# Optimization experiments

Hardware: AMD Instinct MI355X
Metric: run time of the kernel (lower is better)

The kernel has to match this reference:

```python
import jax, jax.numpy as jnp
import numpy as np

N_NODES = 8192
IN_FEATS, H_FEATS, NUM_CLASSES = 512, 256, 16


def _glorot(key, shape):
    fan_in, fan_out = shape[0], shape[1]
    limit = float(np.sqrt(6.0 / (fan_in + fan_out)))
    return jax.random.uniform(key, shape, jnp.float32, -limit, limit)


def setup_inputs() -> dict:
    key = jax.random.key(0)
    ks = jax.random.split(key, 16)
    return {
        "x": jax.random.normal(ks[0], (N_NODES, IN_FEATS), jnp.float32),
        "w1": _glorot(ks[1], (IN_FEATS, H_FEATS)), "b1": jnp.zeros((H_FEATS,), jnp.float32),
        "w2": _glorot(ks[2], (H_FEATS, H_FEATS)), "b2": jnp.zeros((H_FEATS,), jnp.float32),
        "w3": _glorot(ks[3], (H_FEATS, 32)),      "b3": jnp.zeros((32,), jnp.float32),
        "t": _glorot(ks[4], (1, 1)), "theta": _glorot(ks[5], (1, 1)),
        "gw1": _glorot(ks[6], (32, 16)), "gb1": jnp.zeros((16,), jnp.float32),
        "gw2": _glorot(ks[7], (16, 8)),  "gb2": jnp.zeros((8,), jnp.float32),
        "lw1": _glorot(ks[8], (8, 16)),  "lb1": jnp.zeros((16,), jnp.float32),
        "lw2": _glorot(ks[9], (16, NUM_CLASSES)), "lb2": jnp.zeros((NUM_CLASSES,), jnp.float32),
    }


def _pairwise_dist(h):
    # Euclidean cdist(h, h): [N, N], stable sqrt with zero subgradient at d=0
    sq = jnp.sum(h * h, axis=1)
    d2 = jnp.maximum(sq[:, None] + sq[None, :] - 2.0 * (h @ h.T), 0.0)
    return jnp.where(d2 > 0.0, jnp.sqrt(jnp.where(d2 > 0.0, d2, 1.0)), 0.0)


def reference(x, w1, b1, w2, b2, w3, b3, t, theta, gw1, gb1, gw2, gb2, lw1, lb1, lw2, lb2):
    n = x.shape[0]
    # MLP encoder (dropout is eval-mode identity)
    h = jax.nn.relu(x @ w1 + b1)
    h = jax.nn.relu(h @ w2 + b2)
    h = h @ w3 + b3                                  # [N, 32]
    # latent dense graph: A = sigmoid(t * (cdist + theta)); all entries > 0 -> fully dense graph
    A = jax.nn.sigmoid(t[0, 0] * (_pairwise_dist(h) + theta[0, 0]))   # [N, N]
    inv_deg = 1.0 / n                                # norm='right', in-degree == N for dense graph
    # GraphConv: dst aggregates sum_src A[src,dst] * (h[src] @ W) then right-normalizes
    h = jax.nn.relu((A.T @ (h @ gw1)) * inv_deg + gb1)   # [N, 16]
    h = jax.nn.relu((A.T @ (h @ gw2)) * inv_deg + gb2)   # [N, 8]
    h = jax.nn.relu(h @ lw1 + lb1)
    return h @ lw2 + lb2                             # [N, num_classes]
```

## Files before the change

kernel.cpp:

```cpp
#include <hip/hip_runtime.h>

typedef __attribute__((ext_vector_type(8))) short short8;
typedef __attribute__((ext_vector_type(4))) float f32x4;
typedef __attribute__((ext_vector_type(4))) unsigned short u16x4;
typedef unsigned short u16;
typedef unsigned int u32;

#define MFMA16 __builtin_amdgcn_mfma_f32_16x16x32_bf16

__device__ __forceinline__ u16 f2bf(float f) {
    u32 u = __builtin_bit_cast(u32, f);
    return (u16)((u + 0x7FFFu + ((u >> 16) & 1u)) >> 16);
}

__device__ __forceinline__ void split2(float f, u16& hi, u16& lo) {
    u32 u = __builtin_bit_cast(u32, f);
    hi = (u16)(u >> 16);
    float hf = __builtin_bit_cast(float, u & 0xFFFF0000u);
    float r = f - hf;
    lo = (u16)(__builtin_bit_cast(u32, r) >> 16);
}

__device__ __forceinline__ int swzA(int row, int slot) {
    return row * 64 + ((slot ^ ((row >> 1) & 3)) << 4);
}

__global__ void __launch_bounds__(256) k_tr(const float* __restrict__ w, float* __restrict__ wt,
                                            int K, int N) {
    int idx = blockIdx.x * 256 + threadIdx.x;
    if (idx >= K * N) return;
    int k = idx / N, n = idx - k * N;
    wt[n * K + k] = w[idx];
}

template <int K, int BN, bool RELU>
__global__ void __launch_bounds__(256, 2) k_gemm(const float* __restrict__ A,
                                                 const float* __restrict__ Bt,
                                                 const float* __restrict__ bias,
                                                 float* __restrict__ C, const int N) {
    constexpr int NT = BN / 16;
    __shared__ __align__(16) char smem[16384];
    char* const Ah = smem;
    char* const Al = smem + 4096;
    char* const Bh = smem + 8192;
    char* const Bl = smem + 12288;
    const int tid = threadIdx.x, lane = tid & 63, w = tid >> 6;
    const int frow = lane & 15, fg = lane >> 4;
    const int m0 = blockIdx.x * 64, n0 = blockIdx.y * BN;
    const int srow = tid >> 2, sc = tid & 3;
    const int swa = swzA(srow, sc);
    const bool doB = (BN == 64) || (tid < 128);
    const float* gA = A + (m0 + srow) * K + sc * 8;
    const float* gB = Bt + (n0 + srow) * K + sc * 8;

    f32x4 acc[NT];
    float bv[NT];
#pragma unroll
    for (int nt = 0; nt < NT; nt++) {
        acc[nt] = {0.f, 0.f, 0.f, 0.f};
        bv[nt] = bias[n0 + nt * 16 + frow];
    }
    const int fra = swzA(w * 16 + frow, fg);
    int frb[NT];
#pragma unroll
    for (int nt = 0; nt < NT; nt++) frb[nt] = swzA(nt * 16 + frow, fg);

    for (int k0 = 0; k0 < K; k0 += 32) {
        f32x4 a0 = *(const f32x4*)(gA + k0);
        f32x4 a1 = *(const f32x4*)(gA + k0 + 4);
        f32x4 b0 = {0.f, 0.f, 0.f, 0.f}, b1 = {0.f, 0.f, 0.f, 0.f};
        if (doB) {
            b0 = *(const f32x4*)(gB + k0);
            b1 = *(const f32x4*)(gB + k0 + 4);
        }
        __syncthreads();
        {
            short8 ah8, al8;
#pragma unroll
            for (int i = 0; i < 4; i++) { u16 hh, ll; split2(a0[i], hh, ll); ah8[i] = (short)hh; al8[i] = (short)ll; }
#pragma unroll
            for (int i = 0; i < 4; i++) { u16 hh, ll; split2(a1[i], hh, ll); ah8[4 + i] = (short)hh; al8[4 + i] = (short)ll; }
            *(short8*)(Ah + swa) = ah8;
            *(short8*)(Al + swa) = al8;
        }
        if (doB) {
            short8 bh8, bl8;
#pragma unroll
            for (int i = 0; i < 4; i++) { u16 hh, ll; split2(b0[i], hh, ll); bh8[i] = (short)hh; bl8[i] = (short)ll; }
#pragma unroll
            for (int i = 0; i < 4; i++) { u16 hh, ll; split2(b1[i], hh, ll); bh8[4 + i] = (short)hh; bl8[4 + i] = (short)ll; }
            *(short8*)(Bh + swa) = bh8;
            *(short8*)(Bl + swa) = bl8;
        }
        __syncthreads();
        const short8 afh = *(const short8*)(Ah + fra);
        const short8 afl = *(const short8*)(Al + fra);
#pragma unroll
        for (int nt = 0; nt < NT; nt++) {
            const short8 bfh = *(const short8*)(Bh + frb[nt]);
            const short8 bfl = *(const short8*)(Bl + frb[nt]);
            acc[nt] = MFMA16(afh, bfh, acc[nt], 0, 0, 0);
            acc[nt] = MFMA16(afh, bfl, acc[nt], 0, 0, 0);
            acc[nt] = MFMA16(afl, bfh, acc[nt], 0, 0, 0);
        }
    }
#pragma unroll
    for (int nt = 0; nt < NT; nt++) {
#pragma unroll
        for (int r = 0; r < 4; r++) {
            float v = acc[nt][r] + bv[nt];
            if (RELU) v = fmaxf(v, 0.f);
            C[(m0 + w * 16 + fg * 4 + r) * N + (n0 + nt * 16 + frow)] = v;
        }
    }
}

__global__ void __launch_bounds__(256) k_post(const float* __restrict__ H,
                                              const float* __restrict__ gw1,
                                              u16* __restrict__ hhi, u16* __restrict__ hlo,
                                              float* __restrict__ sqv, u16* __restrict__ B1t) {
    __shared__ float gs[512];
    const int tid = threadIdx.x;
    gs[tid] = gw1[tid];
    gs[tid + 256] = gw1[tid + 256];
    __syncthreads();
    const int j = blockIdx.x * 256 + tid;
    float h[32];
#pragma unroll
    for (int q = 0; q < 8; q++) {
        f32x4 v = *(const f32x4*)(H + j * 32 + q * 4);
        h[q * 4 + 0] = v[0]; h[q * 4 + 1] = v[1]; h[q * 4 + 2] = v[2]; h[q * 4 + 3] = v[3];
    }
    float s = 0.f;
#pragma unroll
    for (int k = 0; k < 32; k++) s = fmaf(h[k], h[k], s);
    sqv[j] = s;
#pragma unroll
    for (int q = 0; q < 4; q++) {
        short8 vh, vl;
#pragma unroll
        for (int e = 0; e < 8; e++) {
            u16 hh, ll;
            split2(h[q * 8 + e], hh, ll);
            vh[e] = (short)hh; vl[e] = (short)ll;
        }
        *(short8*)(hhi + j * 32 + q * 8) = vh;
        *(short8*)(hlo + j * 32 + q * 8) = vl;
    }
    const float inv = 0.0001220703125f;
#pragma unroll
    for (int f = 0; f < 16; f++) {
        float a = 0.f;
#pragma unroll
        for (int k = 0; k < 32; k++) a = fmaf(h[k], gs[k * 16 + f], a);
        B1t[f * 8192 + j] = f2bf(a * inv);
    }
}

__global__ void __launch_bounds__(256, 2) k_agg(const u16* __restrict__ hhi,
                                                const u16* __restrict__ hlo,
                                                const float* __restrict__ sqv,
                                                const u16* __restrict__ Bt,
                                                float* __restrict__ P,
                                                const float* __restrict__ tp,
                                                const float* __restrict__ thp) {
    __shared__ __align__(16) char smem[25088];
    const int tid = threadIdx.x;
    const int lane = tid & 63;
    const int w = tid >> 6;
    const int frow = lane & 15, fg = lane >> 4;
    const int dstbase = blockIdx.x * 64;
    const int chunk = blockIdx.y;
    const float t = tp[0], th = thp[0];
    const float c1 = -t * 1.44269504088896340736f;
    const float c0 = c1 * th;

    char* const hdh_p = smem;
    char* const hdl_p = smem + 4096;
    char* const hsh_p = smem + 8192;
    char* const hsl_p = smem + 12288;
    float* const sqd = (float*)(smem + 16384);
    float* const sqs = (float*)(smem + 16640);
    char* const astr = smem + 16896 + w * 2048;

    const int srow = tid >> 2, sc = tid & 3;
    const int swa = swzA(srow, sc);

    {
        short8 vh = *(const short8*)(hhi + (dstbase + srow) * 32 + sc * 8);
        short8 vl = *(const short8*)(hlo + (dstbase + srow) * 32 + sc * 8);
        *(short8*)(hdh_p + swa) = vh;
        *(short8*)(hdl_p + swa) = vl;
        if (tid < 64) sqd[tid] = sqv[dstbase + tid];
    }
    __syncthreads();

    const int fra = swzA(w * 16 + frow, fg);
    const short8 hdh = *(const short8*)(hdh_p + fra);
    const short8 hdl = *(const short8*)(hdl_p + fra);
    const float sq_i = sqd[w * 16 + frow];
    const int il = w * 16 + frow;

    int hsfa[4], aw_off[4], ard[2];
#pragma unroll
    for (int jj = 0; jj < 4; jj++) hsfa[jj] = swzA(jj * 16 + frow, fg);
#pragma unroll
    for (int jj = 0; jj < 4; jj++)
        aw_off[jj] = frow * 128 + (((2 * jj + (fg >> 1)) ^ (frow & 7)) << 4) + ((fg & 1) << 3);
#pragma unroll
    for (int ks = 0; ks < 2; ks++) ard[ks] = frow * 128 + (((4 * ks + fg) ^ (frow & 7)) << 4);

    f32x4 outacc = {0.f, 0.f, 0.f, 0.f};
    const u16* bgp = Bt + frow * 8192;

    for (int jt = chunk * 16; jt < chunk * 16 + 16; ++jt) {
        const int jbase = jt * 64;
        const short8 bf0 = *(const short8*)(bgp + jbase + fg * 8);
        const short8 bf1 = *(const short8*)(bgp + jbase + 32 + fg * 8);
        const short8 vh = *(const short8*)(hhi + (jbase + srow) * 32 + sc * 8);
        const short8 vl = *(const short8*)(hlo + (jbase + srow) * 32 + sc * 8);
        const int il_cmp = (jbase == dstbase) ? il : -1;
        __syncthreads();
        *(short8*)(hsh_p + swa) = vh;
        *(short8*)(hsl_p + swa) = vl;
        if (tid < 64) sqs[tid] = sqv[jbase + tid];
        __syncthreads();

        short8 hsh[4], hsl[4];
#pragma unroll
        for (int jj = 0; jj < 4; jj++) {
            hsh[jj] = *(const short8*)(hsh_p + hsfa[jj]);
            hsl[jj] = *(const short8*)(hsl_p + hsfa[jj]);
        }
        f32x4 sacc[4];
#pragma unroll
        for (int jj = 0; jj < 4; jj++) {
            f32x4 z = {0.f, 0.f, 0.f, 0.f};
            z = MFMA16(hsh[jj], hdh, z, 0, 0, 0);
            z = MFMA16(hsh[jj], hdl, z, 0, 0, 0);
            z = MFMA16(hsl[jj], hdh, z, 0, 0, 0);
            sacc[jj] = z;
        }
#pragma unroll
        for (int jj = 0; jj < 4; jj++) {
            u16x4 av;
#pragma unroll
            for (int r = 0; r < 4; r++) {
                const int jl = jj * 16 + fg * 4 + r;
                const float sqj = sqs[jl];
                float d2 = fmaf(sacc[jj][r], -2.f, sq_i + sqj);
                d2 = fmaxf(d2, 0.f);
                float d = __builtin_amdgcn_sqrtf(d2);
                if (jl == il_cmp) d = 0.f;
                const float zz = fmaf(d, c1, c0);
                const float aa = __builtin_amdgcn_rcpf(1.f + __builtin_amdgcn_exp2f(zz));
                av[r] = f2bf(aa);
            }
            *(u16x4*)(astr + aw_off[jj]) = av;
        }
        const short8 af0 = *(const short8*)(astr + ard[0]);
        const short8 af1 = *(const short8*)(astr + ard[1]);
        outacc = MFMA16(af0, bf0, outacc, 0, 0, 0);
        outacc = MFMA16(af1, bf1, outacc, 0, 0, 0);
    }
#pragma unroll
    for (int r = 0; r < 4; r++) {
        const int ig = dstbase + w * 16 + fg * 4 + r;
        P[(chunk * 8192 + ig) * 16 + frow] = outacc[r];
    }
}

__global__ void __launch_bounds__(256) k_reduce1(const float* __restrict__ P,
                                                 const float* __restrict__ gw2,
                                                 const float* __restrict__ gb1,
                                                 u16* __restrict__ B2t) {
    __shared__ float gs[128];
    const int tid = threadIdx.x;
    if (tid < 128) gs[tid] = gw2[tid];
    __syncthreads();
    const int j = blockIdx.x * 256 + tid;
    float g[16];
#pragma unroll
    for (int q = 0; q < 4; q++) {
        f32x4 v = *(const f32x4*)(P + j * 16 + q * 4);
        g[q * 4 + 0] = v[0]; g[q * 4 + 1] = v[1]; g[q * 4 + 2] = v[2]; g[q * 4 + 3] = v[3];
    }
#pragma unroll
    for (int c = 1; c < 8; c++) {
#pragma unroll
        for (int q = 0; q < 4; q++) {
            f32x4 v = *(const f32x4*)(P + (c * 8192 + j) * 16 + q * 4);
            g[q * 4 + 0] += v[0]; g[q * 4 + 1] += v[1]; g[q * 4 + 2] += v[2]; g[q * 4 + 3] += v[3];
        }
    }
#pragma unroll
    for (int f = 0; f < 16; f++) g[f] = fmaxf(g[f] + gb1[f], 0.f);
    const float inv = 0.0001220703125f;
#pragma unroll
    for (int f2 = 0; f2 < 8; f2++) {
        float a = 0.f;
#pragma unroll
        for (int k = 0; k < 16; k++) a = fmaf(g[k], gs[k * 8 + f2], a);
        B2t[f2 * 8192 + j] = f2bf(a * inv);
    }
#pragma unroll
    for (int f2 = 8; f2 < 16; f2++) B2t[f2 * 8192 + j] = 0;
}

__global__ void __launch_bounds__(256) k_final(const float* __restrict__ P,
                                               const float* __restrict__ gb2,
                                               const float* __restrict__ lw1,
                                               const float* __restrict__ lb1,
                                               const float* __restrict__ lw2,
                                               const float* __restrict__ lb2,
                                               float* __restrict__ out) {
    __shared__ float s1[128], s2[256];
    const int tid = threadIdx.x;
    if (tid < 128) s1[tid] = lw1[tid];
    s2[tid] = lw2[tid];
    __syncthreads();
    const int j = blockIdx.x * 256 + tid;
    float g[8];
#pragma unroll
    for (int q = 0; q < 2; q++) {
        f32x4 v = *(const f32x4*)(P + j * 16 + q * 4);
        g[q * 4 + 0] = v[0]; g[q * 4 + 1] = v[1]; g[q * 4 + 2] = v[2]; g[q * 4 + 3] = v[3];
    }
#pragma unroll
    for (int c = 1; c < 8; c++) {
#pragma unroll
        for (int q = 0; q < 2; q++) {
            f32x4 v = *(const f32x4*)(P + (c * 8192 + j) * 16 + q * 4);
            g[q * 4 + 0] += v[0]; g[q * 4 + 1] += v[1]; g[q * 4 + 2] += v[2]; g[q * 4 + 3] += v[3];
        }
    }
#pragma unroll
    for (int f = 0; f < 8; f++) g[f] = fmaxf(g[f] + gb2[f], 0.f);
    float l1[16];
#pragma unroll
    for (int f = 0; f < 16; f++) {
        float a = lb1[f];
#pragma unroll
        for (int k = 0; k < 8; k++) a = fmaf(g[k], s1[k * 16 + f], a);
        l1[f] = fmaxf(a, 0.f);
    }
#pragma unroll
    for (int q = 0; q < 4; q++) {
        f32x4 v;
#pragma unroll
        for (int e = 0; e < 4; e++) {
            const int f = q * 4 + e;
            float a = lb2[f];
#pragma unroll
            for (int k = 0; k < 16; k++) a = fmaf(l1[k], s2[k * 16 + f], a);
            v[e] = a;
        }
        *(f32x4*)(out + j * 16 + q * 4) = v;
    }
}

extern "C" void kernel_launch(void* const* d_in, const int* in_sizes, int n_in,
                              void* d_out, int out_size, void* d_ws, size_t ws_size,
                              hipStream_t stream) {
    (void)in_sizes; (void)n_in; (void)out_size; (void)ws_size;
    const float* x   = (const float*)d_in[0];
    const float* w1  = (const float*)d_in[1];
    const float* b1  = (const float*)d_in[2];
    const float* w2  = (const float*)d_in[3];
    const float* b2  = (const float*)d_in[4];
    const float* w3  = (const float*)d_in[5];
    const float* b3  = (const float*)d_in[6];
    const float* t   = (const float*)d_in[7];
    const float* th  = (const float*)d_in[8];
    const float* gw1 = (const float*)d_in[9];
    const float* gb1 = (const float*)d_in[10];
    const float* gw2 = (const float*)d_in[11];
    const float* gb2 = (const float*)d_in[12];
    const float* lw1 = (const float*)d_in[13];
    const float* lb1 = (const float*)d_in[14];
    const float* lw2 = (const float*)d_in[15];
    const float* lb2 = (const float*)d_in[16];

    char* ws = (char*)d_ws;
    float* wt1 = (float*)(ws + 0);
    float* wt2 = (float*)(ws + 524288);
    float* wt3 = (float*)(ws + 786432);
    float* H1  = (float*)(ws + 819200);
    float* P   = (float*)(ws + 819200);
    float* H2  = (float*)(ws + 9207808);
    float* H   = (float*)(ws + 17596416);
    u16*   hhi = (u16*)(ws + 18644992);
    u16*   hlo = (u16*)(ws + 19169280);
    float* sqv = (float*)(ws + 19693568);
    u16*   B1t = (u16*)(ws + 19726336);
    u16*   B2t = (u16*)(ws + 19988480);

    k_tr<<<(512 * 256 + 255) / 256, 256, 0, stream>>>(w1, wt1, 512, 256);
    k_tr<<<(256 * 256 + 255) / 256, 256, 0, stream>>>(w2, wt2, 256, 256);
    k_tr<<<(256 * 32 + 255) / 256, 256, 0, stream>>>(w3, wt3, 256, 32);

    k_gemm<512, 64, true ><<<dim3(128, 4), 256, 0, stream>>>(x,  wt1, b1, H1, 256);
    k_gemm<256, 64, true ><<<dim3(128, 4), 256, 0, stream>>>(H1, wt2, b2, H2, 256);
    k_gemm<256, 32, false><<<dim3(128, 1), 256, 0, stream>>>(H2, wt3, b3, H, 32);

    k_post<<<32, 256, 0, stream>>>(H, gw1, hhi, hlo, sqv, B1t);

    k_agg<<<dim3(128, 8), 256, 0, stream>>>(hhi, hlo, sqv, B1t, P, t, th);
    k_reduce1<<<32, 256, 0, stream>>>(P, gw2, gb1, B2t);
    k_agg<<<dim3(128, 8), 256, 0, stream>>>(hhi, hlo, sqv, B2t, P, t, th);
    k_final<<<32, 256, 0, stream>>>(P, gb2, lw1, lb1, lw2, lb2, (float*)d_out);
}
```

Before: 140.1 us.

## Drop LDS staging, pre-split weights/activations to bf16 pairs, double aggregation chunks

The GEMM kernels no longer stage tiles through LDS with barriers. They load MFMA fragments directly from global memory, using weights pre-split into hi/lo bf16 by the transpose kernel and intermediate activations written already split. The aggregation kernel likewise reads source features straight from global memory without syncthreads and packs probabilities with v_cvt_pk_bf16_f32. The source dimension is split into 16 chunks instead of 8 for more parallelism, at the cost of a larger partial-sum reduction and more uncoalesced, L2-dependent global reads.

```diff
diff --git a/kernel.cpp b/kernel.cpp
--- a/kernel.cpp
+++ b/kernel.cpp
@@ -2,11 +2,14 @@
 
 typedef __attribute__((ext_vector_type(8))) short short8;
 typedef __attribute__((ext_vector_type(4))) float f32x4;
-typedef __attribute__((ext_vector_type(4))) unsigned short u16x4;
+typedef __attribute__((ext_vector_type(2))) unsigned int u32x2;
 typedef unsigned short u16;
 typedef unsigned int u32;
 
 #define MFMA16 __builtin_amdgcn_mfma_f32_16x16x32_bf16
+
+constexpr int NCH = 16;
+constexpr int NJT = 8192 / 64 / NCH;
 
 __device__ __forceinline__ u16 f2bf(float f) {
     u32 u = __builtin_bit_cast(u32, f);
@@ -21,38 +24,28 @@
     lo = (u16)(__builtin_bit_cast(u32, r) >> 16);
 }
 
-__device__ __forceinline__ int swzA(int row, int slot) {
-    return row * 64 + ((slot ^ ((row >> 1) & 3)) << 4);
-}
-
-__global__ void __launch_bounds__(256) k_tr(const float* __restrict__ w, float* __restrict__ wt,
-                                            int K, int N) {
+__global__ void __launch_bounds__(256) k_trs(const float* __restrict__ w, u16* __restrict__ wthi,
+                                             u16* __restrict__ wtlo, int K, int N) {
     int idx = blockIdx.x * 256 + threadIdx.x;
     if (idx >= K * N) return;
     int k = idx / N, n = idx - k * N;
-    wt[n * K + k] = w[idx];
-}
-
-template <int K, int BN, bool RELU>
-__global__ void __launch_bounds__(256, 2) k_gemm(const float* __restrict__ A,
-                                                 const float* __restrict__ Bt,
-                                                 const float* __restrict__ bias,
-                                                 float* __restrict__ C, const int N) {
-    constexpr int NT = BN / 16;
-    __shared__ __align__(16) char smem[16384];
-    char* const Ah = smem;
-    char* const Al = smem + 4096;
-    char* const Bh = smem + 8192;
-    char* const Bl = smem + 12288;
+    u16 hh, ll;
+    split2(w[idx], hh, ll);
+    wthi[n * K + k] = hh;
+    wtlo[n * K + k] = ll;
+}
+
+template <int K, int NT, bool RELU, bool AF32, bool OUTSPLIT>
+__global__ void __launch_bounds__(256) k_gemm(const float* __restrict__ Af,
+                                              const u16* __restrict__ Ahi, const u16* __restrict__ Alo,
+                                              const u16* __restrict__ Bthi, const u16* __restrict__ Btlo,
+                                              const float* __restrict__ bias,
+                                              float* __restrict__ Cf, u16* __restrict__ Chi,
+                                              u16* __restrict__ Clo, const int N) {
     const int tid = threadIdx.x, lane = tid & 63, w = tid >> 6;
     const int frow = lane & 15, fg = lane >> 4;
-    const int m0 = blockIdx.x * 64, n0 = blockIdx.y * BN;
-    const int srow = tid >> 2, sc = tid & 3;
-    const int swa = swzA(srow, sc);
-    const bool doB = (BN == 64) || (tid < 128);
-    const float* gA = A + (m0 + srow) * K + sc * 8;
-    const float* gB = Bt + (n0 + srow) * K + sc * 8;
-
+    const int m0 = blockIdx.x * 64, n0 = blockIdx.y * NT * 16;
+    const int arow = m0 + w * 16 + frow;
     f32x4 acc[NT];
     float bv[NT];
 #pragma unroll
@@ -60,48 +53,26 @@
         acc[nt] = {0.f, 0.f, 0.f, 0.f};
         bv[nt] = bias[n0 + nt * 16 + frow];
     }
-    const int fra = swzA(w * 16 + frow, fg);
-    int frb[NT];
-#pragma unroll
-    for (int nt = 0; nt < NT; nt++) frb[nt] = swzA(nt * 16 + frow, fg);
-
     for (int k0 = 0; k0 < K; k0 += 32) {
-        f32x4 a0 = *(const f32x4*)(gA + k0);
-        f32x4 a1 = *(const f32x4*)(gA + k0 + 4);
-        f32x4 b0 = {0.f, 0.f, 0.f, 0.f}, b1 = {0.f, 0.f, 0.f, 0.f};
-        if (doB) {
-            b0 = *(const f32x4*)(gB + k0);
-            b1 = *(const f32x4*)(gB + k0 + 4);
-        }
-        __syncthreads();
-        {
-            short8 ah8, al8;
-#pragma unroll
-            for (int i = 0; i < 4; i++) { u16 hh, ll; split2(a0[i], hh, ll); ah8[i] = (short)hh; al8[i] = (short)ll; }
-#pragma unroll
-            for (int i = 0; i < 4; i++) { u16 hh, ll; split2(a1[i], hh, ll); ah8[4 + i] = (short)hh; al8[4 + i] = (short)ll; }
-            *(short8*)(Ah + swa) = ah8;
-            *(short8*)(Al + swa) = al8;
-        }
-        if (doB) {
-            short8 bh8, bl8;
-#pragma unroll
-            for (int i = 0; i < 4; i++) { u16 hh, ll; split2(b0[i], hh, ll); bh8[i] = (short)hh; bl8[i] = (short)ll; }
-#pragma unroll
-            for (int i = 0; i < 4; i++) { u16 hh, ll; split2(b1[i], hh, ll); bh8[4 + i] = (short)hh; bl8[4 + i] = (short)ll; }
-            *(short8*)(Bh + swa) = bh8;
-            *(short8*)(Bl + swa) = bl8;
-        }
-        __syncthreads();
-        const short8 afh = *(const short8*)(Ah + fra);
-        const short8 afl = *(const short8*)(Al + fra);
+        short8 ah, al;
+        if constexpr (AF32) {
+            const f32x4 a0 = *(const f32x4*)(Af + arow * K + k0 + fg * 8);
+            const f32x4 a1 = *(const f32x4*)(Af + arow * K + k0 + fg * 8 + 4);
+#pragma unroll
+            for (int i = 0; i < 4; i++) { u16 hh, ll; split2(a0[i], hh, ll); ah[i] = (short)hh; al[i] = (short)ll; }
+#pragma unroll
+            for (int i = 0; i < 4; i++) { u16 hh, ll; split2(a1[i], hh, ll); ah[4 + i] = (short)hh; al[4 + i] = (short)ll; }
+        } else {
+            ah = *(const short8*)(Ahi + arow * K + k0 + fg * 8);
+            al = *(const short8*)(Alo + arow * K + k0 + fg * 8);
+        }
 #pragma unroll
         for (int nt = 0; nt < NT; nt++) {
-            const short8 bfh = *(const short8*)(Bh + frb[nt]);
-            const short8 bfl = *(const short8*)(Bl + frb[nt]);
-            acc[nt] = MFMA16(afh, bfh, acc[nt], 0, 0, 0);
-            acc[nt] = MFMA16(afh, bfl, acc[nt], 0, 0, 0);
-            acc[nt] = MFMA16(afl, bfh, acc[nt], 0, 0, 0);
+            const short8 bh = *(const short8*)(Bthi + (n0 + nt * 16 + frow) * K + k0 + fg * 8);
+            const short8 bl = *(const short8*)(Btlo + (n0 + nt * 16 + frow) * K + k0 + fg * 8);
+            acc[nt] = MFMA16(ah, bh, acc[nt], 0, 0, 0);
+            acc[nt] = MFMA16(ah, bl, acc[nt], 0, 0, 0);
+            acc[nt] = MFMA16(al, bh, acc[nt], 0, 0, 0);
         }
     }
 #pragma unroll
@@ -110,7 +81,15 @@
         for (int r = 0; r < 4; r++) {
             float v = acc[nt][r] + bv[nt];
             if (RELU) v = fmaxf(v, 0.f);
-            C[(m0 + w * 16 + fg * 4 + r) * N + (n0 + nt * 16 + frow)] = v;
+            const int row = m0 + w * 16 + fg * 4 + r, col = n0 + nt * 16 + frow;
+            if constexpr (OUTSPLIT) {
+                u16 hh, ll;
+                split2(v, hh, ll);
+                Chi[row * N + col] = hh;
+                Clo[row * N + col] = ll;
+            } else {
+                Cf[row * N + col] = v;
+            }
         }
     }
 }
@@ -157,111 +136,87 @@
     }
 }
 
-__global__ void __launch_bounds__(256, 2) k_agg(const u16* __restrict__ hhi,
-                                                const u16* __restrict__ hlo,
-                                                const float* __restrict__ sqv,
-                                                const u16* __restrict__ Bt,
-                                                float* __restrict__ P,
-                                                const float* __restrict__ tp,
-                                                const float* __restrict__ thp) {
-    __shared__ __align__(16) char smem[25088];
-    const int tid = threadIdx.x;
-    const int lane = tid & 63;
-    const int w = tid >> 6;
+template <bool DIAG>
+__device__ __forceinline__ void ew_pack(char* astr, int awoff, const f32x4 s, const f32x4 sq4,
+                                        float sq_i, float c0, float c1, int jloc, int il) {
+    float p[4];
+#pragma unroll
+    for (int r = 0; r < 4; r++) {
+        float d2 = fmaf(s[r], -2.f, sq_i + sq4[r]);
+        d2 = fmaxf(d2, 0.f);
+        float d = __builtin_amdgcn_sqrtf(d2);
+        if (DIAG) {
+            if (jloc + r == il) d = 0.f;
+        }
+        const float z = fmaf(d, c1, c0);
+        p[r] = __builtin_amdgcn_rcpf(1.f + __builtin_amdgcn_exp2f(z));
+    }
+    u32 w0, w1;
+    asm("v_cvt_pk_bf16_f32 %0, %1, %2" : "=v"(w0) : "v"(p[0]), "v"(p[1]));
+    asm("v_cvt_pk_bf16_f32 %0, %1, %2" : "=v"(w1) : "v"(p[2]), "v"(p[3]));
+    u32x2 pk = {w0, w1};
+    *(u32x2*)(astr + awoff) = pk;
+}
+
+__global__ void __launch_bounds__(256) k_agg(const u16* __restrict__ hhi, const u16* __restrict__ hlo,
+                                             const float* __restrict__ sqv, const u16* __restrict__ Bt,
+                                             float* __restrict__ P,
+                                             const float* __restrict__ tp, const float* __restrict__ thp) {
+    __shared__ __align__(16) char astr_all[8192];
+    const int tid = threadIdx.x, lane = tid & 63, w = tid >> 6;
     const int frow = lane & 15, fg = lane >> 4;
     const int dstbase = blockIdx.x * 64;
     const int chunk = blockIdx.y;
     const float t = tp[0], th = thp[0];
     const float c1 = -t * 1.44269504088896340736f;
     const float c0 = c1 * th;
-
-    char* const hdh_p = smem;
-    char* const hdl_p = smem + 4096;
-    char* const hsh_p = smem + 8192;
-    char* const hsl_p = smem + 12288;
-    float* const sqd = (float*)(smem + 16384);
-    float* const sqs = (float*)(smem + 16640);
-    char* const astr = smem + 16896 + w * 2048;
-
-    const int srow = tid >> 2, sc = tid & 3;
-    const int swa = swzA(srow, sc);
-
-    {
-        short8 vh = *(const short8*)(hhi + (dstbase + srow) * 32 + sc * 8);
-        short8 vl = *(const short8*)(hlo + (dstbase + srow) * 32 + sc * 8);
-        *(short8*)(hdh_p + swa) = vh;
-        *(short8*)(hdl_p + swa) = vl;
-        if (tid < 64) sqd[tid] = sqv[dstbase + tid];
-    }
-    __syncthreads();
-
-    const int fra = swzA(w * 16 + frow, fg);
-    const short8 hdh = *(const short8*)(hdh_p + fra);
-    const short8 hdl = *(const short8*)(hdl_p + fra);
-    const float sq_i = sqd[w * 16 + frow];
+    char* const astr = astr_all + w * 2048;
+
+    const int igf = dstbase + w * 16 + frow;
+    const short8 hdh = *(const short8*)(hhi + igf * 32 + fg * 8);
+    const short8 hdl = *(const short8*)(hlo + igf * 32 + fg * 8);
+    const float sq_i = sqv[igf];
     const int il = w * 16 + frow;
 
-    int hsfa[4], aw_off[4], ard[2];
-#pragma unroll
-    for (int jj = 0; jj < 4; jj++) hsfa[jj] = swzA(jj * 16 + frow, fg);
+    int awo[4], ard[2];
 #pragma unroll
     for (int jj = 0; jj < 4; jj++)
-        aw_off[jj] = frow * 128 + (((2 * jj + (fg >> 1)) ^ (frow & 7)) << 4) + ((fg & 1) << 3);
-#pragma unroll
-    for (int ks = 0; ks < 2; ks++) ard[ks] = frow * 128 + (((4 * ks + fg) ^ (frow & 7)) << 4);
+        awo[jj] = frow * 128 + (((2 * jj + (fg >> 1)) ^ (frow & 7)) << 4) + ((fg & 1) << 3);
+#pragma unroll
+    for (int h = 0; h < 2; h++) ard[h] = frow * 128 + (((4 * h + fg) ^ (frow & 7)) << 4);
 
     f32x4 outacc = {0.f, 0.f, 0.f, 0.f};
-    const u16* bgp = Bt + frow * 8192;
-
-    for (int jt = chunk * 16; jt < chunk * 16 + 16; ++jt) {
-        const int jbase = jt * 64;
-        const short8 bf0 = *(const short8*)(bgp + jbase + fg * 8);
-        const short8 bf1 = *(const short8*)(bgp + jbase + 32 + fg * 8);
-        const short8 vh = *(const short8*)(hhi + (jbase + srow) * 32 + sc * 8);
-        const short8 vl = *(const short8*)(hlo + (jbase + srow) * 32 + sc * 8);
-        const int il_cmp = (jbase == dstbase) ? il : -1;
-        __syncthreads();
-        *(short8*)(hsh_p + swa) = vh;
-        *(short8*)(hsl_p + swa) = vl;
-        if (tid < 64) sqs[tid] = sqv[jbase + tid];
-        __syncthreads();
-
-        short8 hsh[4], hsl[4];
-#pragma unroll
-        for (int jj = 0; jj < 4; jj++) {
-            hsh[jj] = *(const short8*)(hsh_p + hsfa[jj]);
-            hsl[jj] = *(const short8*)(hsl_p + hsfa[jj]);
-        }
-        f32x4 sacc[4];
-#pragma unroll
-        for (int jj = 0; jj < 4; jj++) {
-            f32x4 z = {0.f, 0.f, 0.f, 0.f};
-            z = MFMA16(hsh[jj], hdh, z, 0, 0, 0);
-            z = MFMA16(hsh[jj], hdl, z, 0, 0, 0);
-            z = MFMA16(hsl[jj], hdh, z, 0, 0, 0);
-            sacc[jj] = z;
-        }
-#pragma unroll
-        for (int jj = 0; jj < 4; jj++) {
-            u16x4 av;
-#pragma unroll
-            for (int r = 0; r < 4; r++) {
-                const int jl = jj * 16 + fg * 4 + r;
-                const float sqj = sqs[jl];
-                float d2 = fmaf(sacc[jj][r], -2.f, sq_i + sqj);
-                d2 = fmaxf(d2, 0.f);
-                float d = __builtin_amdgcn_sqrtf(d2);
-                if (jl == il_cmp) d = 0.f;
-                const float zz = fmaf(d, c1, c0);
-                const float aa = __builtin_amdgcn_rcpf(1.f + __builtin_amdgcn_exp2f(zz));
-                av[r] = f2bf(aa);
+
+    for (int jtl = 0; jtl < NJT; ++jtl) {
+        const int jbase = (chunk * NJT + jtl) * 64;
+        const bool diag = (jbase == dstbase);
+#pragma unroll
+        for (int h = 0; h < 2; ++h) {
+            const int sb = jbase + h * 32;
+            const short8 hs0h = *(const short8*)(hhi + (sb + frow) * 32 + fg * 8);
+            const short8 hs0l = *(const short8*)(hlo + (sb + frow) * 32 + fg * 8);
+            const short8 hs1h = *(const short8*)(hhi + (sb + 16 + frow) * 32 + fg * 8);
+            const short8 hs1l = *(const short8*)(hlo + (sb + 16 + frow) * 32 + fg * 8);
+            const f32x4 sq0 = *(const f32x4*)(sqv + sb + fg * 4);
+            const f32x4 sq1 = *(const f32x4*)(sqv + sb + 16 + fg * 4);
+            const short8 bfh = *(const short8*)(Bt + frow * 8192 + sb + fg * 8);
+            f32x4 s0 = {0.f, 0.f, 0.f, 0.f}, s1 = {0.f, 0.f, 0.f, 0.f};
+            s0 = MFMA16(hs0h, hdh, s0, 0, 0, 0);
+            s0 = MFMA16(hs0h, hdl, s0, 0, 0, 0);
+            s0 = MFMA16(hs0l, hdh, s0, 0, 0, 0);
+            s1 = MFMA16(hs1h, hdh, s1, 0, 0, 0);
+            s1 = MFMA16(hs1h, hdl, s1, 0, 0, 0);
+            s1 = MFMA16(hs1l, hdh, s1, 0, 0, 0);
+            if (diag) {
+                ew_pack<true>(astr, awo[2 * h], s0, sq0, sq_i, c0, c1, (2 * h) * 16 + fg * 4, il);
+                ew_pack<true>(astr, awo[2 * h + 1], s1, sq1, sq_i, c0, c1, (2 * h + 1) * 16 + fg * 4, il);
+            } else {
+                ew_pack<false>(astr, awo[2 * h], s0, sq0, sq_i, c0, c1, 0, 0);
+                ew_pack<false>(astr, awo[2 * h + 1], s1, sq1, sq_i, c0, c1, 0, 0);
             }
-            *(u16x4*)(astr + aw_off[jj]) = av;
-        }
-        const short8 af0 = *(const short8*)(astr + ard[0]);
-        const short8 af1 = *(const short8*)(astr + ard[1]);
-        outacc = MFMA16(af0, bf0, outacc, 0, 0, 0);
-        outacc = MFMA16(af1, bf1, outacc, 0, 0, 0);
+            const short8 af = *(const short8*)(astr + ard[h]);
+            outacc = MFMA16(af, bfh, outacc, 0, 0, 0);
+        }
     }
 #pragma unroll
     for (int r = 0; r < 4; r++) {
@@ -286,7 +241,7 @@
         g[q * 4 + 0] = v[0]; g[q * 4 + 1] = v[1]; g[q * 4 + 2] = v[2]; g[q * 4 + 3] = v[3];
     }
 #pragma unroll
-    for (int c = 1; c < 8; c++) {
+    for (int c = 1; c < NCH; c++) {
 #pragma unroll
         for (int q = 0; q < 4; q++) {
             f32x4 v = *(const f32x4*)(P + (c * 8192 + j) * 16 + q * 4);
@@ -327,7 +282,7 @@
         g[q * 4 + 0] = v[0]; g[q * 4 + 1] = v[1]; g[q * 4 + 2] = v[2]; g[q * 4 + 3] = v[3];
     }
 #pragma unroll
-    for (int c = 1; c < 8; c++) {
+    for (int c = 1; c < NCH; c++) {
 #pragma unroll
         for (int q = 0; q < 2; q++) {
             f32x4 v = *(const f32x4*)(P + (c * 8192 + j) * 16 + q * 4);
@@ -382,31 +337,39 @@
     const float* lb2 = (const float*)d_in[16];
 
     char* ws = (char*)d_ws;
-    float* wt1 = (float*)(ws + 0);
-    float* wt2 = (float*)(ws + 524288);
-    float* wt3 = (float*)(ws + 786432);
-    float* H1  = (float*)(ws + 819200);
-    float* P   = (float*)(ws + 819200);
-    float* H2  = (float*)(ws + 9207808);
-    float* H   = (float*)(ws + 17596416);
-    u16*   hhi = (u16*)(ws + 18644992);
-    u16*   hlo = (u16*)(ws + 19169280);
+    u16* wt1h = (u16*)(ws + 0);
+    u16* wt1l = (u16*)(ws + 262144);
+    u16* wt2h = (u16*)(ws + 524288);
+    u16* wt2l = (u16*)(ws + 655360);
+    u16* wt3h = (u16*)(ws + 786432);
+    u16* wt3l = (u16*)(ws + 802816);
+    u16* H1h  = (u16*)(ws + 819200);
+    u16* H1l  = (u16*)(ws + 5013504);
+    float* P  = (float*)(ws + 819200);
+    u16* H2h  = (u16*)(ws + 9207808);
+    u16* H2l  = (u16*)(ws + 13402112);
+    float* H  = (float*)(ws + 17596416);
+    u16* hhi  = (u16*)(ws + 18644992);
+    u16* hlo  = (u16*)(ws + 19169280);
     float* sqv = (float*)(ws + 19693568);
-    u16*   B1t = (u16*)(ws + 19726336);
-    u16*   B2t = (u16*)(ws + 19988480);
-
-    k_tr<<<(512 * 256 + 255) / 256, 256, 0, stream>>>(w1, wt1, 512, 256);
-    k_tr<<<(256 * 256 + 255) / 256, 256, 0, stream>>>(w2, wt2, 256, 256);
-    k_tr<<<(256 * 32 + 255) / 256, 256, 0, stream>>>(w3, wt3, 256, 32);
-
-    k_gemm<512, 64, true ><<<dim3(128, 4), 256, 0, stream>>>(x,  wt1, b1, H1, 256);
-    k_gemm<256, 64, true ><<<dim3(128, 4), 256, 0, stream>>>(H1, wt2, b2, H2, 256);
-    k_gemm<256, 32, false><<<dim3(128, 1), 256, 0, stream>>>(H2, wt3, b3, H, 32);
+    u16* B1t  = (u16*)(ws + 19726336);
+    u16* B2t  = (u16*)(ws + 19988480);
+
+    k_trs<<<512, 256, 0, stream>>>(w1, wt1h, wt1l, 512, 256);
+    k_trs<<<256, 256, 0, stream>>>(w2, wt2h, wt2l, 256, 256);
+    k_trs<<<32, 256, 0, stream>>>(w3, wt3h, wt3l, 256, 32);
+
+    k_gemm<512, 4, true, true, true><<<dim3(128, 4), 256, 0, stream>>>(
+        x, nullptr, nullptr, wt1h, wt1l, b1, nullptr, H1h, H1l, 256);
+    k_gemm<256, 4, true, false, true><<<dim3(128, 4), 256, 0, stream>>>(
+        nullptr, H1h, H1l, wt2h, wt2l, b2, nullptr, H2h, H2l, 256);
+    k_gemm<256, 2, false, false, false><<<dim3(128, 1), 256, 0, stream>>>(
+        nullptr, H2h, H2l, wt3h, wt3l, b3, H, nullptr, nullptr, 32);
 
     k_post<<<32, 256, 0, stream>>>(H, gw1, hhi, hlo, sqv, B1t);
 
-    k_agg<<<dim3(128, 8), 256, 0, stream>>>(hhi, hlo, sqv, B1t, P, t, th);
+    k_agg<<<dim3(128, NCH), 256, 0, stream>>>(hhi, hlo, sqv, B1t, P, t, th);
     k_reduce1<<<32, 256, 0, stream>>>(P, gw2, gb1, B2t);
-    k_agg<<<dim3(128, 8), 256, 0, stream>>>(hhi, hlo, sqv, B2t, P, t, th);
+    k_agg<<<dim3(128, NCH), 256, 0, stream>>>(hhi, hlo, sqv, B2t, P, t, th);
     k_final<<<32, 256, 0, stream>>>(P, gb2, lw1, lb1, lw2, lb2, (float*)d_out);
 }
```

Measured after the change: 222.7 us. +59.0%, slower.
